# Optimization experiments

Hardware: AMD Instinct MI355X
Metric: run time of the kernel (lower is better)

Reference implementation:

```python
import jax, jax.numpy as jnp
import numpy as np

B, H, W, Q, E, M, K, WIN = 4, 192, 192, 160, 96, 96, 4, 7
NO_ELECTRON_WEIGHT = 0.1


def _bce_logits(x, z):
    # binary_cross_entropy_with_logits, elementwise: softplus(x) - x*z
    return jnp.logaddexp(0.0, x) - x * z


def setup_inputs() -> dict:
    key = jax.random.key(0)
    ks = jax.random.split(key, 11)
    is_electron_logit = jax.random.normal(ks[0], (B * Q,), jnp.float32)
    true_segmap = jax.random.uniform(ks[1], (B, H, W, E), jnp.float32)
    binary_mask_logits = jax.random.normal(ks[2], (B, H, W, Q), jnp.float32)
    portion_logits = jax.random.normal(ks[3], (B, H, W, Q), jnp.float32)
    # keep incidence points away from borders so the 7x7 window stays in-bounds
    incidence_points = jax.random.uniform(ks[4], (B, E, 2), jnp.float32) * (H - 8) + 4.0
    positions = jax.random.uniform(ks[5], (B, Q, 2), jnp.float32) * H
    a = jax.random.normal(ks[6], (B, Q, 3), jnp.float32)
    l00 = jax.nn.softplus(a[..., 0]) + 0.1
    l11 = jax.nn.softplus(a[..., 2]) + 0.1
    l10 = 0.5 * a[..., 1]
    zero = jnp.zeros_like(l00)
    chol = jnp.stack([jnp.stack([l00, zero], -1), jnp.stack([l10, l11], -1)], -2)  # [B,Q,2,2] lower-tri
    occupancy_logits = jax.random.normal(ks[7], (B, H, W, K), jnp.float32)
    occupancy_true = jax.random.randint(ks[8], (B, H, W), 0, K, jnp.int32)
    qkeys = jax.random.split(ks[9], B)
    matched_q = jnp.stack([jax.random.permutation(k, Q)[:M] for k in qkeys]).astype(jnp.int32)
    ekeys = jax.random.split(ks[10], B)
    matched_e = jnp.stack([jax.random.permutation(k, E) for k in ekeys]).astype(jnp.int32)
    return dict(is_electron_logit=is_electron_logit, true_segmap=true_segmap,
                binary_mask_logits=binary_mask_logits, portion_logits=portion_logits,
                incidence_points=incidence_points, positions=positions, chol=chol,
                occupancy_logits=occupancy_logits, occupancy_true=occupancy_true,
                matched_q=matched_q, matched_e=matched_e)


def reference(is_electron_logit, true_segmap, binary_mask_logits, portion_logits,
              incidence_points, positions, chol, occupancy_logits, occupancy_true,
              matched_q, matched_e):
    # ---- class loss (weighted BCE over flat per-query logits) ----
    labels = jnp.zeros((B * Q,), is_electron_logit.dtype)
    glob = (jnp.arange(B)[:, None] * Q + matched_q).reshape(-1)
    labels = labels.at[glob].set(1.0)
    weights = jnp.where(labels > 0, 1.0, NO_ELECTRON_WEIGHT).astype(is_electron_logit.dtype)
    class_loss = jnp.mean(weights * _bce_logits(is_electron_logit, labels))

    # ---- reorder segmentation maps to matched order (_reorder_segmentation_map) ----
    true_r = jnp.take_along_axis(true_segmap, matched_e[:, None, None, :], axis=3)        # [B,H,W,M]
    bin_r = jnp.take_along_axis(binary_mask_logits, matched_q[:, None, None, :], axis=3)  # [B,H,W,M]
    por_r = jnp.take_along_axis(portion_logits, matched_q[:, None, None, :], axis=3)      # [B,H,W,M]

    # ---- mask BCE on 7x7 windows around floor(matched incidence point) ----
    pts_r = jnp.take_along_axis(incidence_points, matched_e[..., None], axis=1)  # [B,M,2]
    pix = jnp.floor(pts_r).astype(jnp.int32)
    half = WIN // 2
    dr = jnp.arange(-half, half + 1)
    rows = pix[..., 0][:, :, None, None] + dr[None, None, :, None]  # [B,M,7,1]
    cols = pix[..., 1][:, :, None, None] + dr[None, None, None, :]  # [B,M,1,7]
    bi = jnp.arange(B)[:, None, None, None]
    mi = jnp.arange(M)[None, :, None, None]
    tv = true_r[bi, rows, cols, mi]  # [B,M,7,7]
    lg = bin_r[bi, rows, cols, mi]
    bce_loss = jnp.mean(_bce_logits(lg, tv))

    # ---- dice loss (softmax over matched-electron dim) ----
    portion = jax.nn.softmax(por_r, axis=-1)
    num = jnp.sum(2.0 * true_r * portion, axis=(1, 2, 3))
    den = jnp.sum(true_r + portion, axis=(1, 2, 3))
    dice_loss = jnp.mean(1.0 - (num + 1.0) / (den + 1.0))

    # ---- distance NLL (2D MVN with lower-tri scale) ----
    centers_r = jnp.take_along_axis(positions, matched_q[..., None], axis=1)       # [B,M,2]
    chol_r = jnp.take_along_axis(chol, matched_q[..., None, None], axis=1)         # [B,M,2,2]
    d = pts_r - centers_r
    z0 = d[..., 0] / chol_r[..., 0, 0]
    z1 = (d[..., 1] - chol_r[..., 1, 0] * z0) / chol_r[..., 1, 1]
    nll = 0.5 * (z0 * z0 + z1 * z1) + jnp.log(2.0 * jnp.pi) \
          + jnp.log(chol_r[..., 0, 0]) + jnp.log(chol_r[..., 1, 1])
    nll = jnp.where(jnp.isinf(nll), 1e7, nll)
    nll_loss = jnp.mean(nll)

    # ---- occupancy loss (per-pixel electron-count cross-entropy) ----
    logp = jax.nn.log_softmax(occupancy_logits, axis=-1)
    occ_loss = -jnp.mean(jnp.take_along_axis(logp, occupancy_true[..., None], axis=-1))

    # loss_weights all 1.0 (defaults); dot(weights, terms)
    return class_loss + bce_loss + dice_loss + nll_loss + occ_loss
```

## Files before the change

kernel.cpp:

```cpp
#include <hip/hip_runtime.h>
#include <math.h>

#define B_ 4
#define H_ 192
#define W_ 192
#define Q_ 160
#define E_ 96
#define M_ 96
#define HW_ (H_ * W_)
#define NPIX_ (B_ * HW_)
#define TPIX 8
#define NJOB 36
#define NDICE 1024
#define NSMALL 962
#define NBUCKET 64
#define WS_NUM0 4
#define WS_TS0  260
#define WS_TOTAL 516

template <int CTRL, int RMASK>
__device__ __forceinline__ float dpp_add_step(float x) {
    int v = __builtin_amdgcn_update_dpp(0, __float_as_int(x), CTRL, RMASK, 0xF, false);
    return x + __int_as_float(v);
}
__device__ __forceinline__ float wave_sum63(float x) {
    x = dpp_add_step<0x111, 0xF>(x);
    x = dpp_add_step<0x112, 0xF>(x);
    x = dpp_add_step<0x114, 0xF>(x);
    x = dpp_add_step<0x118, 0xF>(x);
    x = dpp_add_step<0x142, 0xA>(x);
    x = dpp_add_step<0x143, 0xC>(x);
    return x;
}

__device__ __forceinline__ float waveSumAll(float v) {
    for (int m = 32; m > 0; m >>= 1) v += __shfl_xor(v, m, 64);
    return v;
}

__device__ __forceinline__ float softplusf(float x) {
    return fmaxf(x, 0.f) + log1pf(__expf(-fabsf(x)));
}

__global__ __launch_bounds__(256) void fused_kernel(
    const float* __restrict__ logit,
    const float* __restrict__ trueseg,
    const float* __restrict__ binlog,
    const float* __restrict__ por,
    const float* __restrict__ inc,
    const float* __restrict__ pos,
    const float* __restrict__ chol,
    const float* __restrict__ occlog,
    const int* __restrict__ occtrue,
    const int* __restrict__ mqall,
    const int* __restrict__ meall,
    float* __restrict__ ws)
{
    __shared__ float lab[B_ * Q_];
    const int tid  = threadIdx.x;
    const int lane = tid & 63;
    const int wid  = tid >> 6;
    const int blk  = blockIdx.x;

    if (blk < NDICE) {
        const int b = blk >> 8;
        const int slot = blk & 255;
        const bool hi = lane < 32;
        const int* mq = mqall + b * M_;
        const int* me = meall + b * M_;
        const int mqa = mq[lane];
        const int mea = me[lane];
        int mqb = 0, meb = 0;
        if (hi) { mqb = mq[64 + lane]; meb = me[64 + lane]; }
        const float m1 = hi ? 1.f : 0.f;

        const float* porb = por + (size_t)b * HW_ * Q_;
        const float* trb  = trueseg + (size_t)b * HW_ * E_;

        float an = 0.f;
        float at = 0.f;

        #pragma unroll 4
        for (int j = 0; j < NJOB; ++j) {
            const int pix = (slot + (j >> 1) * 256) * TPIX + wid * 2 + (j & 1);
            const float* pr = porb + (size_t)pix * Q_;
            const float* tr = trb  + (size_t)pix * E_;
            float p0v = pr[mqa];
            float t0  = tr[mea];
            float p1  = pr[mqb];
            float t1  = tr[meb];
            float e0 = __expf(p0v);
            float e1 = __expf(p1) * m1;
            float s  = wave_sum63(e0 + e1);
            float se = wave_sum63(fmaf(t1, e1, t0 * e0));
            an += __fdividef(se, s);
            at += fmaf(t1, m1, t0);
        }

        float atr = wave_sum63(at);
        if (lane == 63) {
            int bucket = blk & (NBUCKET - 1);
            atomicAdd(&ws[WS_NUM0 + bucket * 4 + b], 2.f * an);
            atomicAdd(&ws[WS_TS0  + bucket * 4 + b], atr);
        }
    } else {
        const int s = blk - NDICE;
        float acc = 0.f;
        if (s == 0) {
            for (int i = tid; i < B_ * Q_; i += 256) lab[i] = 0.f;
            __syncthreads();
            for (int i = tid; i < B_ * M_; i += 256) {
                int b = i / M_;
                lab[b * Q_ + mqall[i]] = 1.f;
            }
            __syncthreads();
            for (int i = tid; i < B_ * Q_; i += 256) {
                float x = logit[i];
                float z = lab[i];
                float w = z > 0.f ? 1.f : 0.1f;
                acc += w * (softplusf(x) - x * z);
            }
            float wsum = wave_sum63(acc);
            if (lane == 63) atomicAdd(&ws[0], wsum);
        } else if (s == 1) {
            for (int i = tid; i < B_ * M_; i += 256) {
                int b = i / M_;
                int qi = mqall[i];
                int ei = meall[i];
                float px = inc[(b * E_ + ei) * 2 + 0];
                float py = inc[(b * E_ + ei) * 2 + 1];
                float cx = pos[(b * Q_ + qi) * 2 + 0];
                float cy = pos[(b * Q_ + qi) * 2 + 1];
                const float* ch = chol + (size_t)(b * Q_ + qi) * 4;
                float l00 = ch[0], l10 = ch[2], l11 = ch[3];
                float d0 = px - cx, d1 = py - cy;
                float z0 = d0 / l00;
                float z1 = (d1 - l10 * z0) / l11;
                float nll = 0.5f * (z0 * z0 + z1 * z1) + 1.837877066409345f
                            + logf(l00) + logf(l11);
                if (isinf(nll)) nll = 1e7f;
                acc += nll;
            }
            float wsum = wave_sum63(acc);
            if (lane == 63) atomicAdd(&ws[2], wsum);
        } else if (s < 386) {
            int idx = s - 2;
            int b = idx / M_;
            int ei = meall[idx];
            int qi = mqall[idx];
            float px = inc[(b * E_ + ei) * 2 + 0];
            float py = inc[(b * E_ + ei) * 2 + 1];
            int r0 = (int)floorf(px) - 3;
            int c0 = (int)floorf(py) - 3;
            if (tid < 49) {
                int rr = r0 + tid / 7;
                int cc = c0 + tid % 7;
                size_t pix = ((size_t)b * H_ + rr) * W_ + cc;
                float tv = trueseg[pix * E_ + ei];
                float lg = binlog[pix * Q_ + qi];
                acc = softplusf(lg) - lg * tv;
            }
            if (wid == 0) {
                float wsum = wave_sum63(acc);
                if (lane == 63) atomicAdd(&ws[1], wsum);
            }
        } else {
            int p = (s - 386) * 256 + tid;
            if (p < NPIX_) {
                float4 v = *(const float4*)(occlog + (size_t)p * 4);
                int lb = occtrue[p];
                float m = fmaxf(fmaxf(v.x, v.y), fmaxf(v.z, v.w));
                float lse = m + __logf(__expf(v.x - m) + __expf(v.y - m) +
                                       __expf(v.z - m) + __expf(v.w - m));
                float xs = lb == 0 ? v.x : (lb == 1 ? v.y : (lb == 2 ? v.z : v.w));
                acc = lse - xs;
            }
            float wsum = wave_sum63(acc);
            if (lane == 63) atomicAdd(&ws[3], wsum);
        }
    }
}

__global__ __launch_bounds__(64) void final_kernel(const float* __restrict__ ws,
                                                   float* __restrict__ out)
{
    const int lane = threadIdx.x;
    float n[B_], t[B_];
    for (int b = 0; b < B_; ++b) {
        n[b] = waveSumAll(ws[WS_NUM0 + lane * 4 + b]);
        t[b] = waveSumAll(ws[WS_TS0  + lane * 4 + b]);
    }
    if (lane == 0) {
        float class_l = ws[0] * (1.f / (B_ * Q_));
        float bce_l   = ws[1] * (1.f / (B_ * M_ * 49));
        float nll_l   = ws[2] * (1.f / (B_ * M_));
        float occ_l   = ws[3] * (1.f / NPIX_);
        float dice = 0.f;
        for (int b = 0; b < B_; ++b)
            dice += 1.f - (n[b] + 1.f) / (t[b] + (float)HW_ + 1.f);
        dice *= (1.f / B_);
        out[0] = class_l + bce_l + nll_l + occ_l + dice;
    }
}

extern "C" void kernel_launch(void* const* d_in, const int* in_sizes, int n_in,
                              void* d_out, int out_size, void* d_ws, size_t ws_size,
                              hipStream_t stream) {
    const float* logit   = (const float*)d_in[0];
    const float* trueseg = (const float*)d_in[1];
    const float* binlog  = (const float*)d_in[2];
    const float* por     = (const float*)d_in[3];
    const float* inc     = (const float*)d_in[4];
    const float* pos     = (const float*)d_in[5];
    const float* chol    = (const float*)d_in[6];
    const float* occlog  = (const float*)d_in[7];
    const int*   occtrue = (const int*)d_in[8];
    const int*   mq      = (const int*)d_in[9];
    const int*   me      = (const int*)d_in[10];
    float* out = (float*)d_out;
    float* ws  = (float*)d_ws;

    (void)hipMemsetAsync(d_ws, 0, WS_TOTAL * sizeof(float), stream);

    hipLaunchKernelGGL(fused_kernel, dim3(NDICE + NSMALL), dim3(256), 0, stream,
                       logit, trueseg, binlog, por, inc, pos, chol, occlog, occtrue,
                       mq, me, ws);
    hipLaunchKernelGGL(final_kernel, dim3(1), dim3(64), 0, stream, ws, out);
}
```

Baseline: 260.2 us.

## Stage dice pixel tiles into LDS with async global_load_lds multi-buffering

Replaces the per-pixel scattered global gathers in the dice blocks with contiguous 16-byte global-to-LDS async copies of whole 8-pixel tiles (portion and true rows). A four-slot ring buffer is prefetched three tiles ahead, with explicit vmcnt waits and barriers, and the gathers then read from LDS. The aim is to turn random row accesses into coalesced streaming and to overlap memory latency with compute. In exchange it adds 32 KB of LDS per block, which may reduce occupancy, plus a barrier per tile. It also loads whole rows, including the unmatched columns the old gathers never touched.

New measurement: 262.7 us. No clear change (+0.9%).

```diff
diff --git a/kernel.cpp b/kernel.cpp
--- a/kernel.cpp
+++ b/kernel.cpp
@@ -10,13 +10,21 @@
 #define HW_ (H_ * W_)
 #define NPIX_ (B_ * HW_)
 #define TPIX 8
-#define NJOB 36
+#define NTILE 18
+#define NBUF 4
+#define TILE_B 8192
 #define NDICE 1024
 #define NSMALL 962
 #define NBUCKET 64
 #define WS_NUM0 4
 #define WS_TS0  260
 #define WS_TOTAL 516
+
+__device__ __forceinline__ void stage16(const void* g, void* l) {
+    __builtin_amdgcn_global_load_lds(
+        (const __attribute__((address_space(1))) void*)g,
+        (__attribute__((address_space(3))) void*)l, 16, 0, 0);
+}
 
 template <int CTRL, int RMASK>
 __device__ __forceinline__ float dpp_add_step(float x) {
@@ -56,7 +64,7 @@
     const int* __restrict__ meall,
     float* __restrict__ ws)
 {
-    __shared__ float lab[B_ * Q_];
+    __shared__ float tilebuf[NBUF * TILE_B / 4];
     const int tid  = threadIdx.x;
     const int lane = tid & 63;
     const int wid  = tid >> 6;
@@ -66,36 +74,79 @@
         const int b = blk >> 8;
         const int slot = blk & 255;
         const bool hi = lane < 32;
+        const int l31 = lane & 31;
         const int* mq = mqall + b * M_;
         const int* me = meall + b * M_;
         const int mqa = mq[lane];
         const int mea = me[lane];
-        int mqb = 0, meb = 0;
-        if (hi) { mqb = mq[64 + lane]; meb = me[64 + lane]; }
+        const int mqb = mq[64 + l31];
+        const int meb = me[64 + l31];
         const float m1 = hi ? 1.f : 0.f;
 
-        const float* porb = por + (size_t)b * HW_ * Q_;
-        const float* trb  = trueseg + (size_t)b * HW_ * E_;
+        const char* porb = (const char*)(por + (size_t)b * HW_ * Q_);
+        const char* trb  = (const char*)(trueseg + (size_t)b * HW_ * E_);
+
+        asm volatile("s_waitcnt vmcnt(0)" ::: "memory");
 
         float an = 0.f;
         float at = 0.f;
 
+        #define STAGE(t_) do {                                                 \
+            const int p0_ = (slot + (t_) * 256) * TPIX;                        \
+            const char* gp_ = porb + (size_t)p0_ * (Q_ * 4);                   \
+            const char* gt_ = trb  + (size_t)p0_ * (E_ * 4);                   \
+            char* dst_ = (char*)tilebuf + ((t_) & (NBUF - 1)) * TILE_B;        \
+            const int o0_ = wid * 1024;                                        \
+            const char* s0_ = (o0_ < 5120) ? (gp_ + o0_) : (gt_ + o0_ - 5120); \
+            stage16(s0_ + lane * 16, dst_ + o0_);                              \
+            const int o1_ = o0_ + 4096;                                        \
+            const char* s1_ = (o1_ < 5120) ? (gp_ + o1_) : (gt_ + o1_ - 5120); \
+            stage16(s1_ + lane * 16, dst_ + o1_);                              \
+        } while (0)
+
+        #define COMP(t_) do {                                                  \
+            const float* pl_ = tilebuf + ((t_) & (NBUF - 1)) * (TILE_B / 4);   \
+            const float* tl_ = pl_ + TPIX * Q_;                                \
+            _Pragma("unroll")                                                  \
+            for (int k = 0; k < 2; ++k) {                                      \
+                const int pix_ = wid * 2 + k;                                  \
+                float p0v_ = pl_[pix_ * Q_ + mqa];                             \
+                float t0_  = tl_[pix_ * E_ + mea];                             \
+                float p1_  = pl_[pix_ * Q_ + mqb];                             \
+                float t1_  = tl_[pix_ * E_ + meb];                             \
+                float e0_ = __expf(p0v_);                                      \
+                float e1_ = __expf(p1_) * m1;                                  \
+                float s_  = wave_sum63(e0_ + e1_);                             \
+                float se_ = wave_sum63(fmaf(t1_, e1_, t0_ * e0_));             \
+                an += __fdividef(se_, s_);                                     \
+                at += fmaf(t1_, m1, t0_);                                      \
+            }                                                                  \
+        } while (0)
+
+        STAGE(0); STAGE(1); STAGE(2);
+
         #pragma unroll 4
-        for (int j = 0; j < NJOB; ++j) {
-            const int pix = (slot + (j >> 1) * 256) * TPIX + wid * 2 + (j & 1);
-            const float* pr = porb + (size_t)pix * Q_;
-            const float* tr = trb  + (size_t)pix * E_;
-            float p0v = pr[mqa];
-            float t0  = tr[mea];
-            float p1  = pr[mqb];
-            float t1  = tr[meb];
-            float e0 = __expf(p0v);
-            float e1 = __expf(p1) * m1;
-            float s  = wave_sum63(e0 + e1);
-            float se = wave_sum63(fmaf(t1, e1, t0 * e0));
-            an += __fdividef(se, s);
-            at += fmaf(t1, m1, t0);
+        for (int t = 0; t < NTILE - 2; ++t) {
+            asm volatile("s_waitcnt vmcnt(4)" ::: "memory");
+            asm volatile("s_waitcnt lgkmcnt(0)" ::: "memory");
+            __builtin_amdgcn_s_barrier();
+            __builtin_amdgcn_sched_barrier(0);
+            if (t + 3 < NTILE) STAGE(t + 3);
+            COMP(t);
         }
+        asm volatile("s_waitcnt vmcnt(2)" ::: "memory");
+        asm volatile("s_waitcnt lgkmcnt(0)" ::: "memory");
+        __builtin_amdgcn_s_barrier();
+        __builtin_amdgcn_sched_barrier(0);
+        COMP(NTILE - 2);
+        asm volatile("s_waitcnt vmcnt(0)" ::: "memory");
+        asm volatile("s_waitcnt lgkmcnt(0)" ::: "memory");
+        __builtin_amdgcn_s_barrier();
+        __builtin_amdgcn_sched_barrier(0);
+        COMP(NTILE - 1);
+
+        #undef STAGE
+        #undef COMP
 
         float atr = wave_sum63(at);
         if (lane == 63) {
@@ -104,6 +155,7 @@
             atomicAdd(&ws[WS_TS0  + bucket * 4 + b], atr);
         }
     } else {
+        float* lab = tilebuf;
         const int s = blk - NDICE;
         float acc = 0.f;
         if (s == 0) {
```
